# Kernel tuning notes

Hardware: AMD Instinct MI355X
Metric: run time of the kernel (lower is better)

The kernel has to match this reference:

```python
import jax, jax.numpy as jnp
import numpy as np

NUM_EMB = 8192
EMB_DIM = 512
SPAN = 8            # max_span == fixed_segment_size
COMMIT = 0.25
BOUND_W = 0.01


def setup_inputs() -> dict:
    key = jax.random.key(0)
    k_x, k_e, k_w = jax.random.split(key, 3)
    B, T, D = 16, 8192, EMB_DIM
    x = jax.random.normal(k_x, (B, T, D), dtype=jnp.float32)
    emb = jax.random.normal(k_e, (NUM_EMB, D), dtype=jnp.float32) * 0.02
    Wb = jax.random.normal(k_w, (D, 1), dtype=jnp.float32) * 0.02
    bb = jnp.zeros((1,), dtype=jnp.float32)
    return {"x": x, "emb": emb, "Wb": Wb, "bb": bb}


def reference(x, emb, Wb, bb):
    # Eval-mode forward of AdaptiveTemporalVQ (no gumbel sampling, no EMA update).
    B, T, D = x.shape
    # boundary predictor: Linear(D, 1) -> squeeze
    boundary_logits = (x @ Wb)[..., 0] + bb[0]                      # [B, T]
    boundaries = (jax.nn.sigmoid(boundary_logits) > 0.5).astype(x.dtype)

    num_segments = (T + SPAN - 1) // SPAN
    pad = num_segments * SPAN - T
    x_p = jnp.pad(x, ((0, 0), (0, pad), (0, 0))) if pad > 0 else x
    # temporal mean pooling over fixed segments
    pooled = x_p.reshape(B, num_segments, SPAN, D).mean(axis=2)      # [B, S, D]

    # --- VectorQuantizer ---
    flat = pooled.reshape(-1, D)                                     # [N, D]
    dist = (jnp.sum(flat ** 2, axis=1, keepdims=True)
            + jnp.sum(emb ** 2, axis=1)
            - 2.0 * flat @ emb.T)                                    # [N, K]
    idx = jnp.argmin(dist, axis=1)                                   # [N]
    quantized = emb[idx].reshape(B, num_segments, D)                 # codebook gather

    e_latent_loss = jnp.mean((jax.lax.stop_gradient(quantized) - pooled) ** 2)
    vq_loss = COMMIT * e_latent_loss
    # straight-through estimator
    q_st = pooled + jax.lax.stop_gradient(quantized - pooled)

    # expand each segment code back over its SPAN timesteps
    q_exp = jnp.broadcast_to(q_st[:, :, None, :], (B, num_segments, SPAN, D))
    quantized_out = q_exp.reshape(B, num_segments * SPAN, D)[:, :T, :]
    idx_seg = idx.reshape(B, num_segments)
    idx_out = jnp.broadcast_to(idx_seg[:, :, None], (B, num_segments, SPAN))
    idx_out = idx_out.reshape(B, num_segments * SPAN)[:, :T]

    target_rate = jnp.float32(1.0 / SPAN)
    boundary_loss = (boundaries.mean() - target_rate) ** 2
    total_loss = vq_loss + BOUND_W * boundary_loss
    return quantized_out, total_loss, idx_out, boundaries
```

## Files before the change

### kernel.cpp

```cpp
#include <hip/hip_runtime.h>

#define B_    16
#define T_    8192
#define D_    512
#define K_    8192
#define S_    1024
#define N_    16384
#define NBT   131072

#define LOSS_OFF 67108864
#define IDX_OFF  67108865
#define BND_OFF  67239937

typedef __bf16 bf16x8 __attribute__((ext_vector_type(8)));
typedef float  f32x4  __attribute__((ext_vector_type(4)));

__device__ __forceinline__ unsigned int fsort(float f){
  unsigned int u = __float_as_uint(f);
  return (u & 0x80000000u) ? ~u : (u | 0x80000000u);
}
__device__ __forceinline__ float funsort(unsigned int su){
  unsigned int u = (su & 0x80000000u) ? (su ^ 0x80000000u) : ~su;
  return __uint_as_float(u);
}
__device__ __forceinline__ unsigned short f2bf(float f){
  unsigned int u = __float_as_uint(f);
  return (unsigned short)((u + 0x7fffu + ((u >> 16) & 1u)) >> 16);
}
__device__ __forceinline__ void gload16(const void* g, void* l){
  __builtin_amdgcn_global_load_lds((const __attribute__((address_space(1))) void*)g,
                                   (__attribute__((address_space(3))) void*)l, 16, 0, 0);
}

__global__ void k_embnorm(const float4* __restrict__ emb4, float* __restrict__ enorm,
                          unsigned short* __restrict__ embh, int* __restrict__ cnt){
  if(blockIdx.x == 0 && threadIdx.x == 0) *cnt = 0;
  const int wid  = (blockIdx.x * blockDim.x + threadIdx.x) >> 6;
  const int lane = threadIdx.x & 63;
  float4 a = emb4[wid * 128 + (lane << 1)];
  float4 b = emb4[wid * 128 + (lane << 1) + 1];
  float s = a.x*a.x + a.y*a.y + a.z*a.z + a.w*a.w
          + b.x*b.x + b.y*b.y + b.z*b.z + b.w*b.w;
  #pragma unroll
  for(int off = 32; off; off >>= 1) s += __shfl_xor(s, off);
  if(lane == 0) enorm[wid] = s;
  unsigned short* dst = embh + ((size_t)wid << 9) + (lane << 3);
  *(ushort4*)(dst)     = make_ushort4(f2bf(a.x), f2bf(a.y), f2bf(a.z), f2bf(a.w));
  *(ushort4*)(dst + 4) = make_ushort4(f2bf(b.x), f2bf(b.y), f2bf(b.z), f2bf(b.w));
}

__launch_bounds__(256)
__global__ void k_prep(const float4* __restrict__ x4, const float4* __restrict__ wb4,
                       const float* __restrict__ bb, float4* __restrict__ pooled4,
                       unsigned short* __restrict__ pooledh, float* __restrict__ bnd,
                       int* __restrict__ cnt){
  __shared__ double ld[4][8][8];
  const int tid  = threadIdx.x;
  const int row0 = blockIdx.x << 5;
  const double bbv = (double)bb[0];
  #pragma unroll
  for(int it = 0; it < 2; it++){
    const int slot  = (it << 8) + tid;
    const int seg_l = slot >> 7;
    const int c4    = slot & 127;
    const float4 w  = wb4[c4];
    const float4* src = x4 + ((size_t)(row0 + (seg_l << 3)) * 128 + c4);
    float4 acc = src[0];
    double p[8];
    p[0] = (double)acc.x*w.x + (double)acc.y*w.y + (double)acc.z*w.z + (double)acc.w*w.w;
    #pragma unroll
    for(int t = 1; t < 8; t++){
      const float4 v = src[(size_t)t * 128];
      acc.x += v.x; acc.y += v.y; acc.z += v.z; acc.w += v.w;
      p[t] = (double)v.x*w.x + (double)v.y*w.y + (double)v.z*w.z + (double)v.w*w.w;
    }
    acc.x *= 0.125f; acc.y *= 0.125f; acc.z *= 0.125f; acc.w *= 0.125f;
    const int u = ((blockIdx.x << 2) + seg_l) * 128 + c4;
    pooled4[u] = acc;
    *(ushort4*)(pooledh + ((size_t)u << 2)) =
        make_ushort4(f2bf(acc.x), f2bf(acc.y), f2bf(acc.z), f2bf(acc.w));
    #pragma unroll
    for(int t = 0; t < 8; t++){
      #pragma unroll
      for(int off = 1; off < 16; off <<= 1) p[t] += __shfl_xor(p[t], off);
    }
    if((c4 & 15) == 0){
      #pragma unroll
      for(int t = 0; t < 8; t++) ld[seg_l][t][c4 >> 4] = p[t];
    }
  }
  __syncthreads();
  if(tid < 32){
    const double* q = ld[tid >> 3][tid & 7];
    double s = bbv;
    #pragma unroll
    for(int h = 0; h < 8; h++) s += q[h];
    const bool f = s > 0.0;
    bnd[row0 + tid] = f ? 1.0f : 0.0f;
    const unsigned long long m = __ballot(f);
    if(tid == 0) atomicAdd(cnt, (int)__popcll(m));
  }
}

__launch_bounds__(256, 4)
__global__ void k_distx(const unsigned short* __restrict__ Ah,
                        const unsigned short* __restrict__ Bh,
                        const float* __restrict__ enorm,
                        unsigned long long* __restrict__ cand64){
  __shared__ __align__(16) unsigned short sA[4096];
  __shared__ __align__(16) unsigned short sB[4096];
  const int tid  = threadIdx.x;
  const int w    = tid >> 6, lane = tid & 63;
  const int wm   = w >> 1,  wn   = w & 1;
  const int c    = lane & 15, q  = lane >> 4;

  const int bid   = blockIdx.x;
  const int xcd   = bid & 7;
  const int local = bid >> 3;
  const int row_t = (xcd << 4) + (local & 15);
  const int col_t = local >> 4;
  const int rowbase = row_t << 7;
  const int colbase = col_t << 7;

  f32x4 acc[4][4];
  #pragma unroll
  for(int i = 0; i < 4; i++)
    #pragma unroll
    for(int j = 0; j < 4; j++) acc[i][j] = (f32x4){0.f, 0.f, 0.f, 0.f};

  const int sr  = lane >> 2;
  const int skc = (lane & 3) << 3;

  const unsigned short* Ap0 = Ah + (size_t)(rowbase + w*32 + sr)      * 512 + skc;
  const unsigned short* Ap1 = Ah + (size_t)(rowbase + w*32 + 16 + sr) * 512 + skc;
  const unsigned short* Bp0 = Bh + (size_t)(colbase + w*32 + sr)      * 512 + skc;
  const unsigned short* Bp1 = Bh + (size_t)(colbase + w*32 + 16 + sr) * 512 + skc;
  unsigned short* lA0 = &sA[(w*32)      * 32];
  unsigned short* lA1 = &sA[(w*32 + 16) * 32];
  unsigned short* lB0 = &sB[(w*32)      * 32];
  unsigned short* lB1 = &sB[(w*32 + 16) * 32];

  for(int kb = 0; kb < 512; kb += 32){
    gload16(Ap0 + kb, lA0);
    gload16(Ap1 + kb, lA1);
    gload16(Bp0 + kb, lB0);
    gload16(Bp1 + kb, lB1);
    __syncthreads();
    bf16x8 af[4], bg[4];
    #pragma unroll
    for(int i = 0; i < 4; i++) af[i] = *(const bf16x8*)&sA[(wm*64 + i*16 + c)*32 + q*8];
    #pragma unroll
    for(int j = 0; j < 4; j++) bg[j] = *(const bf16x8*)&sB[(wn*64 + j*16 + c)*32 + q*8];
    #pragma unroll
    for(int i = 0; i < 4; i++)
      #pragma unroll
      for(int j = 0; j < 4; j++)
        acc[i][j] = __builtin_amdgcn_mfma_f32_16x16x32_bf16(af[i], bg[j], acc[i][j], 0, 0, 0);
    __syncthreads();
  }

  float en[4];
  #pragma unroll
  for(int j = 0; j < 4; j++) en[j] = enorm[colbase + wn*64 + j*16 + c];

  #pragma unroll
  for(int i = 0; i < 4; i++){
    #pragma unroll
    for(int r = 0; r < 4; r++){
      unsigned int k1 = 0xffffffffu, k2 = 0xffffffffu;
      #pragma unroll
      for(int j = 0; j < 4; j++){
        const float d = fmaf(-2.0f, acc[i][j][r], en[j]);
        const unsigned int col = (unsigned int)(colbase + wn*64 + j*16 + c);
        const unsigned int key = (fsort(d) & 0xffffe000u) | col;
        if(key < k1){ k2 = k1; k1 = key; } else if(key < k2){ k2 = key; }
      }
      #pragma unroll
      for(int off = 1; off < 16; off <<= 1){
        const unsigned int o1 = __shfl_xor(k1, off);
        const unsigned int o2 = __shfl_xor(k2, off);
        if(o1 < k1){ k2 = min(k1, o2); k1 = o1; }
        else       { k2 = min(k2, o1); }
      }
      if(c == 0){
        const int row = rowbase + wm*64 + i*16 + (q << 2) + r;
        cand64[((size_t)row << 7) + (col_t << 1) + wn] =
            ((unsigned long long)k2 << 32) | k1;
      }
    }
  }
}

__launch_bounds__(256)
__global__ void k_fixup(const float* __restrict__ pooled, const float* __restrict__ emb,
                        const unsigned long long* __restrict__ cand64,
                        int* __restrict__ idxf, double* __restrict__ part){
  const int lane = threadIdx.x & 63, wv = threadIdx.x >> 6;
  const int row = (blockIdx.x << 2) + wv;
  const ulonglong2* cr = (const ulonglong2*)(cand64 + ((size_t)row << 7));
  const ulonglong2 v = cr[lane];
  unsigned int ks[4];
  ks[0] = (unsigned int)v.x; ks[1] = (unsigned int)(v.x >> 32);
  ks[2] = (unsigned int)v.y; ks[3] = (unsigned int)(v.y >> 32);
  unsigned int mn = min(min(ks[0], ks[1]), min(ks[2], ks[3]));
  #pragma unroll
  for(int off = 32; off; off >>= 1) mn = min(mn, (unsigned int)__shfl_xor(mn, off));
  const float thr = funsort(mn & 0xffffe000u) + 0.01f;

  double bestd = 1e300; int besti = 0x7fffffff;
  const float4* p4 = (const float4*)(pooled + ((size_t)row << 9));
  const float4 pa = p4[lane << 1], pb = p4[(lane << 1) + 1];
  #pragma unroll
  for(int g = 0; g < 4; g++){
    const bool flag = funsort(ks[g] & 0xffffe000u) <= thr;
    unsigned long long mask = __ballot(flag);
    while(mask){
      const int l = __ffsll(mask) - 1;
      mask &= mask - 1;
      const int code = (int)(__shfl(ks[g], l) & 0x1fffu);
      const float4* e4 = (const float4*)(emb + ((size_t)code << 9));
      const float4 ea = e4[lane << 1], eb = e4[(lane << 1) + 1];
      double s = 0.0, d;
      d = (double)pa.x - ea.x; s += d * d;  d = (double)pa.y - ea.y; s += d * d;
      d = (double)pa.z - ea.z; s += d * d;  d = (double)pa.w - ea.w; s += d * d;
      d = (double)pb.x - eb.x; s += d * d;  d = (double)pb.y - eb.y; s += d * d;
      d = (double)pb.z - eb.z; s += d * d;  d = (double)pb.w - eb.w; s += d * d;
      #pragma unroll
      for(int off = 32; off; off >>= 1) s += __shfl_xor(s, off);
      if(s < bestd || (s == bestd && code < besti)){ bestd = s; besti = code; }
    }
  }
  __shared__ double se[4];
  if(lane == 0){ idxf[row] = besti; se[wv] = bestd; }
  __syncthreads();
  if(threadIdx.x == 0) part[blockIdx.x] = se[0] + se[1] + se[2] + se[3];
}

__global__ void k_loss(const double* __restrict__ part, const int* __restrict__ cnt,
                       float* __restrict__ out_loss){
  const int tid = threadIdx.x;
  double s = 0.0;
  for(int i = tid; i < 4096; i += 256) s += part[i];
  #pragma unroll
  for(int off = 32; off; off >>= 1) s += __shfl_xor(s, off);
  __shared__ double sb[4];
  if((tid & 63) == 0) sb[tid >> 6] = s;
  __syncthreads();
  if(tid == 0){
    const double e  = sb[0] + sb[1] + sb[2] + sb[3];
    const double el = e / (double)((size_t)N_ * 512);
    const double bm = (double)(*cnt) / 131072.0 - 0.125;
    const double loss = 0.25 * el + 0.01 * bm * bm;
    *out_loss = (float)loss;
  }
}

__launch_bounds__(256)
__global__ void k_expand(const float4* __restrict__ emb4, const int* __restrict__ idxf,
                         float4* __restrict__ q4, float* __restrict__ idxo){
  const int lane = threadIdx.x & 63, wv = threadIdx.x >> 6;
  const int seg = (blockIdx.x << 2) + wv;
  const int idx = idxf[seg];
  const float4 a = emb4[idx * 128 + (lane << 1)];
  const float4 b = emb4[idx * 128 + (lane << 1) + 1];
  float4* dst = q4 + ((size_t)seg << 10);
  #pragma unroll
  for(int t = 0; t < 8; t++){
    dst[t * 128 + (lane << 1)]     = a;
    dst[t * 128 + (lane << 1) + 1] = b;
  }
  if(lane < 8) idxo[(seg << 3) + lane] = (float)idx;
}

extern "C" void kernel_launch(void* const* d_in, const int* in_sizes, int n_in,
                              void* d_out, int out_size, void* d_ws, size_t ws_size,
                              hipStream_t stream){
  const float* x   = (const float*)d_in[0];
  const float* emb = (const float*)d_in[1];
  const float* wb  = (const float*)d_in[2];
  const float* bb  = (const float*)d_in[3];
  float* out = (float*)d_out;

  char* ws = (char*)d_ws;
  int*    cnt   = (int*)(ws + 0);
  double* part  = (double*)(ws + 64);
  float*  enorm = (float*)(ws + 32832);
  int*    idxf  = (int*)(ws + 65600);

  float*              pooled  = (float*)d_out;
  unsigned long long* cand64  = (unsigned long long*)((char*)d_out + (48ull  << 20));
  unsigned short*     pooledh = (unsigned short*)((char*)d_out + (80ull  << 20));
  unsigned short*     embh    = (unsigned short*)((char*)d_out + (100ull << 20));

  float* bnd   = out + BND_OFF;
  float* idxo  = out + IDX_OFF;
  float* lossp = out + LOSS_OFF;

  hipLaunchKernelGGL(k_embnorm, dim3(2048),  dim3(256), 0, stream, (const float4*)emb, enorm, embh, cnt);
  hipLaunchKernelGGL(k_prep,    dim3(4096),  dim3(256), 0, stream, (const float4*)x, (const float4*)wb,
                     bb, (float4*)pooled, pooledh, bnd, cnt);
  hipLaunchKernelGGL(k_distx,   dim3(8192),  dim3(256), 0, stream, pooledh, embh, enorm, cand64);
  hipLaunchKernelGGL(k_fixup,   dim3(4096),  dim3(256), 0, stream, pooled, emb, cand64, idxf, part);
  hipLaunchKernelGGL(k_loss,    dim3(1),     dim3(256), 0, stream, part, cnt, lossp);
  hipLaunchKernelGGL(k_expand,  dim3(4096),  dim3(256), 0, stream, (const float4*)emb, idxf, (float4*)d_out, idxo);
}
```

Before: 700.4 us.

## Enlarge distance GEMM tiles and add 4-stage async LDS pipeline with swizzle

The bf16 distance GEMM now uses 256x256 tiles with 512-thread blocks, so each wave computes a 128x64 sub-tile. A 4-deep ring of LDS buffers is filled with global_load_lds and gated by explicit vmcnt waits and barriers, which lets loads for later k-steps overlap MFMA work on the current one. The LDS layout is XOR-swizzled to reduce bank conflicts, and setprio raises priority around the MFMA block. In exchange it uses 128KB of LDS per block and more accumulator registers, which limits occupancy to one block per CU, and it writes four column candidates per tile instead of two.

```diff
diff --git a/kernel.cpp b/kernel.cpp
--- a/kernel.cpp
+++ b/kernel.cpp
@@ -31,6 +31,13 @@
   __builtin_amdgcn_global_load_lds((const __attribute__((address_space(1))) void*)g,
                                    (__attribute__((address_space(3))) void*)l, 16, 0, 0);
 }
+
+#define VMW12() asm volatile("s_waitcnt vmcnt(12)" ::: "memory")
+#define VMW8()  asm volatile("s_waitcnt vmcnt(8)"  ::: "memory")
+#define VMW4()  asm volatile("s_waitcnt vmcnt(4)"  ::: "memory")
+#define VMW0()  asm volatile("s_waitcnt vmcnt(0)"  ::: "memory")
+#define LGKW()  asm volatile("s_waitcnt lgkmcnt(0)" ::: "memory")
+#define BAR()   asm volatile("s_barrier" ::: "memory")
 
 __global__ void k_embnorm(const float4* __restrict__ emb4, float* __restrict__ enorm,
                           unsigned short* __restrict__ embh, int* __restrict__ cnt){
@@ -102,69 +109,92 @@
   }
 }
 
-__launch_bounds__(256, 4)
+__launch_bounds__(512)
 __global__ void k_distx(const unsigned short* __restrict__ Ah,
                         const unsigned short* __restrict__ Bh,
                         const float* __restrict__ enorm,
                         unsigned long long* __restrict__ cand64){
-  __shared__ __align__(16) unsigned short sA[4096];
-  __shared__ __align__(16) unsigned short sB[4096];
+  __shared__ __align__(16) unsigned short smem[65536];
+
   const int tid  = threadIdx.x;
   const int w    = tid >> 6, lane = tid & 63;
-  const int wm   = w >> 1,  wn   = w & 1;
+  const int wm   = w >> 2,  wn   = w & 3;
   const int c    = lane & 15, q  = lane >> 4;
 
   const int bid   = blockIdx.x;
   const int xcd   = bid & 7;
   const int local = bid >> 3;
-  const int row_t = (xcd << 4) + (local & 15);
-  const int col_t = local >> 4;
-  const int rowbase = row_t << 7;
-  const int colbase = col_t << 7;
-
-  f32x4 acc[4][4];
-  #pragma unroll
-  for(int i = 0; i < 4; i++)
+  const int row_t = (xcd << 3) + (local & 7);
+  const int col_t = local >> 3;
+  const int rowbase = row_t << 8;
+  const int colbase = col_t << 8;
+
+  f32x4 acc[8][4];
+  #pragma unroll
+  for(int i = 0; i < 8; i++)
     #pragma unroll
     for(int j = 0; j < 4; j++) acc[i][j] = (f32x4){0.f, 0.f, 0.f, 0.f};
 
-  const int sr  = lane >> 2;
-  const int skc = (lane & 3) << 3;
-
-  const unsigned short* Ap0 = Ah + (size_t)(rowbase + w*32 + sr)      * 512 + skc;
-  const unsigned short* Ap1 = Ah + (size_t)(rowbase + w*32 + 16 + sr) * 512 + skc;
-  const unsigned short* Bp0 = Bh + (size_t)(colbase + w*32 + sr)      * 512 + skc;
-  const unsigned short* Bp1 = Bh + (size_t)(colbase + w*32 + 16 + sr) * 512 + skc;
-  unsigned short* lA0 = &sA[(w*32)      * 32];
-  unsigned short* lA1 = &sA[(w*32 + 16) * 32];
-  unsigned short* lB0 = &sB[(w*32)      * 32];
-  unsigned short* lB1 = &sB[(w*32 + 16) * 32];
-
-  for(int kb = 0; kb < 512; kb += 32){
-    gload16(Ap0 + kb, lA0);
-    gload16(Ap1 + kb, lA1);
-    gload16(Bp0 + kb, lB0);
-    gload16(Bp1 + kb, lB1);
-    __syncthreads();
-    bf16x8 af[4], bg[4];
-    #pragma unroll
-    for(int i = 0; i < 4; i++) af[i] = *(const bf16x8*)&sA[(wm*64 + i*16 + c)*32 + q*8];
-    #pragma unroll
-    for(int j = 0; j < 4; j++) bg[j] = *(const bf16x8*)&sB[(wn*64 + j*16 + c)*32 + q*8];
-    #pragma unroll
-    for(int i = 0; i < 4; i++)
-      #pragma unroll
-      for(int j = 0; j < 4; j++)
-        acc[i][j] = __builtin_amdgcn_mfma_f32_16x16x32_bf16(af[i], bg[j], acc[i][j], 0, 0, 0);
-    __syncthreads();
-  }
+  const int sr  = tid >> 2;
+  const int cg  = (((tid & 3) ^ ((tid >> 3) & 3)) << 3);
+  const int wbase = w << 9;
+
+  const unsigned short* As0 = Ah + (size_t)(rowbase + sr)       * 512 + cg;
+  const unsigned short* As1 = Ah + (size_t)(rowbase + 128 + sr) * 512 + cg;
+  const unsigned short* Bs0 = Bh + (size_t)(colbase + sr)       * 512 + cg;
+  const unsigned short* Bs1 = Bh + (size_t)(colbase + 128 + sr) * 512 + cg;
+
+  const int ch = ((q ^ ((c >> 1) & 3)) << 3);
+
+  #define STAGE(tt) do{                                                   \
+    const int bb_ = ((tt) & 3) << 14;                                     \
+    const size_t ko_ = (size_t)(tt) << 5;                                 \
+    gload16(As0 + ko_, &smem[bb_ + wbase]);                               \
+    gload16(As1 + ko_, &smem[bb_ + 4096  + wbase]);                       \
+    gload16(Bs0 + ko_, &smem[bb_ + 8192  + wbase]);                       \
+    gload16(Bs1 + ko_, &smem[bb_ + 12288 + wbase]);                       \
+  }while(0)
+
+  #define COMPUTE(tt) do{                                                 \
+    const int bb_ = ((tt) & 3) << 14;                                     \
+    bf16x8 af[8], bg[4];                                                  \
+    _Pragma("unroll")                                                     \
+    for(int i = 0; i < 8; i++)                                            \
+      af[i] = *(const bf16x8*)&smem[bb_ + (wm*128 + i*16 + c)*32 + ch];   \
+    _Pragma("unroll")                                                     \
+    for(int j = 0; j < 4; j++)                                            \
+      bg[j] = *(const bf16x8*)&smem[bb_ + 8192 + (wn*64 + j*16 + c)*32 + ch]; \
+    __builtin_amdgcn_s_setprio(1);                                        \
+    _Pragma("unroll")                                                     \
+    for(int i = 0; i < 8; i++)                                            \
+      _Pragma("unroll")                                                   \
+      for(int j = 0; j < 4; j++)                                          \
+        acc[i][j] = __builtin_amdgcn_mfma_f32_16x16x32_bf16(af[i], bg[j], acc[i][j], 0, 0, 0); \
+    __builtin_amdgcn_s_setprio(0);                                        \
+  }while(0)
+
+  STAGE(0); STAGE(1); STAGE(2);
+
+  #pragma unroll 1
+  for(int t = 0; t < 13; ++t){
+    STAGE(t + 3);
+    VMW12(); BAR();
+    COMPUTE(t);
+    LGKW(); BAR();
+  }
+  VMW8(); BAR(); COMPUTE(13); LGKW(); BAR();
+  VMW4(); BAR(); COMPUTE(14); LGKW(); BAR();
+  VMW0(); BAR(); COMPUTE(15);
+
+  #undef STAGE
+  #undef COMPUTE
 
   float en[4];
   #pragma unroll
   for(int j = 0; j < 4; j++) en[j] = enorm[colbase + wn*64 + j*16 + c];
 
   #pragma unroll
-  for(int i = 0; i < 4; i++){
+  for(int i = 0; i < 8; i++){
     #pragma unroll
     for(int r = 0; r < 4; r++){
       unsigned int k1 = 0xffffffffu, k2 = 0xffffffffu;
@@ -183,8 +213,8 @@
         else       { k2 = min(k2, o1); }
       }
       if(c == 0){
-        const int row = rowbase + wm*64 + i*16 + (q << 2) + r;
-        cand64[((size_t)row << 7) + (col_t << 1) + wn] =
+        const int row = rowbase + wm*128 + i*16 + (q << 2) + r;
+        cand64[((size_t)row << 7) + (col_t << 2) + wn] =
             ((unsigned long long)k2 << 32) | k1;
       }
     }
@@ -299,7 +329,7 @@
   hipLaunchKernelGGL(k_embnorm, dim3(2048),  dim3(256), 0, stream, (const float4*)emb, enorm, embh, cnt);
   hipLaunchKernelGGL(k_prep,    dim3(4096),  dim3(256), 0, stream, (const float4*)x, (const float4*)wb,
                      bb, (float4*)pooled, pooledh, bnd, cnt);
-  hipLaunchKernelGGL(k_distx,   dim3(8192),  dim3(256), 0, stream, pooledh, embh, enorm, cand64);
+  hipLaunchKernelGGL(k_distx,   dim3(2048),  dim3(512), 0, stream, pooledh, embh, enorm, cand64);
   hipLaunchKernelGGL(k_fixup,   dim3(4096),  dim3(256), 0, stream, pooled, emb, cand64, idxf, part);
   hipLaunchKernelGGL(k_loss,    dim3(1),     dim3(256), 0, stream, part, cnt, lossp);
   hipLaunchKernelGGL(k_expand,  dim3(4096),  dim3(256), 0, stream, (const float4*)emb, idxf, (float4*)d_out, idxo);
```

After: 710.9 us. Within noise of the previous version (+1.5%).
